# Performance work log

Hardware: AMD Instinct MI355X
Metric: run time of the kernel (lower is better)

Reference implementation:

```python
import jax, jax.numpy as jnp
import numpy as np

N_NODES = 20000
N_EDGES = 320000
NFEAT = 50
ALPHA = 0.2  # leaky relu slope
EPS = 1e-16


def _gat_head(x, src, dst, W, a, concat):
    # x: (N, Fin), W: (Fin, Fout), a: (2*Fout,)
    N = x.shape[0]
    Wh = x @ W                      # (N, Fout)
    Fout = W.shape[1]
    # edge_h @ a == Wh[src] @ a[:Fout] + Wh[dst] @ a[Fout:]
    s_src = Wh @ a[:Fout]           # (N,)
    s_dst = Wh @ a[Fout:]           # (N,)
    e = jax.nn.leaky_relu(s_src[src] + s_dst[dst], negative_slope=ALPHA)  # (E,)
    # segment softmax over incoming edges of each target node
    e_max = jax.ops.segment_max(e, dst, num_segments=N)   # (N,)
    e_exp = jnp.exp(e - e_max[dst])                         # (E,)
    e_sum = jax.ops.segment_sum(e_exp, dst, num_segments=N)
    att = e_exp / (e_sum[dst] + EPS)                        # (E,)
    msg = Wh[src] * att[:, None]                            # (E, Fout)
    h = jax.ops.segment_sum(msg, dst, num_segments=N)       # (N, Fout)
    return jax.nn.elu(h) if concat else h


def _multi_head(x, src, dst, W, a, concat):
    # W: (H, Fin, Fout), a: (H, 2*Fout) -> (H, N, Fout)
    return jax.vmap(_gat_head, in_axes=(None, None, None, 0, 0, None))(x, src, dst, W, a, concat)


def setup_inputs() -> dict:
    key = jax.random.key(0)
    ks = jax.random.split(key, 8)
    x = jax.random.normal(ks[0], (N_NODES, NFEAT), dtype=jnp.float32)
    edge_index = jax.random.randint(ks[1], (2, N_EDGES), 0, N_NODES, dtype=jnp.int64)
    s = 0.1
    W1 = jax.random.normal(ks[2], (4, NFEAT, 256), dtype=jnp.float32) * s
    a1 = jax.random.normal(ks[3], (4, 512), dtype=jnp.float32) * s
    W2 = jax.random.normal(ks[4], (4, 1024, 256), dtype=jnp.float32) * s
    a2 = jax.random.normal(ks[5], (4, 512), dtype=jnp.float32) * s
    W3 = jax.random.normal(ks[6], (6, 1024, 121), dtype=jnp.float32) * s
    a3 = jax.random.normal(ks[7], (6, 242), dtype=jnp.float32) * s
    return {"x": x, "edge_index": edge_index, "W1": W1, "a1": a1, "W2": W2, "a2": a2, "W3": W3, "a3": a3}


def reference(x, edge_index, W1, a1, W2, a2, W3, a3):
    src, dst = edge_index[0], edge_index[1]
    N = x.shape[0]
    # layer 1: 4 heads, concat -> (N, 1024), then elu
    h1 = _multi_head(x, src, dst, W1, a1, True)      # (4, N, 256)
    x1 = jnp.transpose(h1, (1, 0, 2)).reshape(N, -1)  # concat along feature dim
    x1 = jax.nn.elu(x1)
    # layer 2: 4 heads, concat + skip connection, then elu
    h2 = _multi_head(x1, src, dst, W2, a2, True)
    x2 = jnp.transpose(h2, (1, 0, 2)).reshape(N, -1)
    x2 = jax.nn.elu(x2 + x1)
    # layer 3: 6 heads, no concat-elu, mean over heads
    h3 = _multi_head(x2, src, dst, W3, a3, False)     # (6, N, 121)
    x3 = jnp.mean(h3, axis=0)
    return jax.nn.sigmoid(x3)
```

## Files before the change

kernel.cpp:

```cpp
#include <hip/hip_runtime.h>
#include <cstdint>

#define N_NODES 20000
#define N_EDGES 320000
#define ALPHA 0.2f
#define GAT_EPS 1e-16f
#define MPAD 20096
#define RBLK 157
#define RHI 20
#define SCAN_BLKS 80
#define BT_ROWS 1152

typedef __attribute__((ext_vector_type(8))) _Float16 half8;
typedef __attribute__((ext_vector_type(4))) _Float16 half4t;
typedef __attribute__((ext_vector_type(16))) float f32x16;
typedef __attribute__((ext_vector_type(2))) float f32x2;

__device__ __forceinline__ float elu1(float x) { return x > 0.f ? x : __expf(x) - 1.f; }

__device__ __forceinline__ unsigned char f2fp8(float x) {
    return (unsigned char)(__builtin_amdgcn_cvt_pk_fp8_f32(x, 0.f, 0, false) & 0xff);
}

__device__ __forceinline__ void async16(const void* g, void* l) {
    __builtin_amdgcn_global_load_lds(
        (const __attribute__((address_space(1))) unsigned int*)g,
        (__attribute__((address_space(3))) unsigned int*)l, 16, 0, 0);
}

__device__ __forceinline__ float rdlanef(float v, int j) {
    return __int_as_float(__builtin_amdgcn_readlane(__float_as_int(v), j));
}

__global__ void hist_kernel(const int* __restrict__ dst, int* __restrict__ counts, int E) {
    int e = blockIdx.x * blockDim.x + threadIdx.x;
    if (e < E) atomicAdd(&counts[dst[e]], 1);
}

__global__ void scan1_kernel(const int* __restrict__ counts, int* __restrict__ excl,
                             int* __restrict__ partial, int N) {
    __shared__ int sh[256];
    int t = threadIdx.x, b = blockIdx.x;
    int i = b * 256 + t;
    int v = (i < N) ? counts[i] : 0;
    sh[t] = v;
    __syncthreads();
    for (int d = 1; d < 256; d <<= 1) {
        int x = (t >= d) ? sh[t - d] : 0;
        __syncthreads();
        sh[t] += x;
        __syncthreads();
    }
    if (i < N) excl[i] = sh[t] - v;
    if (t == 255) partial[b] = sh[255];
}

__global__ void scan2_kernel(int* __restrict__ partial) {
    __shared__ int sh[128];
    int t = threadIdx.x;
    int v = (t < SCAN_BLKS) ? partial[t] : 0;
    sh[t] = v;
    __syncthreads();
    for (int d = 1; d < 128; d <<= 1) {
        int x = (t >= d) ? sh[t - d] : 0;
        __syncthreads();
        sh[t] += x;
        __syncthreads();
    }
    if (t < SCAN_BLKS) partial[t] = sh[t] - v;
}

__global__ void scan3_kernel(const int* __restrict__ excl, const int* __restrict__ partial,
                             int* __restrict__ rowptr, int* __restrict__ cursor, int N, int E) {
    int t = threadIdx.x, b = blockIdx.x;
    int i = b * 256 + t;
    if (i < N) {
        int v = excl[i] + partial[b];
        rowptr[i] = v;
        cursor[i] = v;
    }
    if (i == 0) rowptr[N] = E;
}

__global__ void scatter_kernel(const int* __restrict__ src, const int* __restrict__ dst,
                               int* __restrict__ cursor, int* __restrict__ esrc, int E) {
    int e = blockIdx.x * blockDim.x + threadIdx.x;
    if (e < E) {
        int p = atomicAdd(&cursor[dst[e]], 1);
        esrc[p] = src[e];
    }
}

__global__ void pack_x16(const float* __restrict__ x, _Float16* __restrict__ A) {
    int idx = blockIdx.x * 256 + threadIdx.x;
    int r = idx >> 6, c = idx & 63;
    float v = (r < N_NODES && c < 50) ? x[r * 50 + c] : 0.f;
    A[idx] = (_Float16)v;
}

__global__ void pack_bt1(const float* __restrict__ W, _Float16* __restrict__ Bt) {
    int idx = blockIdx.x * 256 + threadIdx.x;
    int c = idx >> 6, k = idx & 63;
    int h = c >> 8, f = c & 255;
    float v = (k < 50) ? W[((size_t)h * 50 + k) * 256 + f] : 0.f;
    Bt[idx] = (_Float16)v;
}

__global__ void pack_bt16(const float* __restrict__ W, _Float16* __restrict__ Bt,
                          int F, int Fpad, int Ctot) {
    int c = blockIdx.y;
    int k = blockIdx.x * blockDim.x + threadIdx.x;
    float v = 0.f;
    if (c < Ctot) {
        int h = c / Fpad, f = c - h * Fpad;
        if (f < F) v = W[(size_t)h * 1024 * F + (size_t)k * F + f];
    }
    Bt[(size_t)c * 1024 + k] = (_Float16)v;
}

__global__ __launch_bounds__(64) void wtilde_kernel(const float* __restrict__ W,
                                                    const float* __restrict__ a,
                                                    _Float16* __restrict__ BT, int Kreal,
                                                    int Kdim, int F, int H, int Nfeat) {
    int k = blockIdx.x, j = blockIdx.y;
    if (j >= 2 * H) return;
    int lane = threadIdx.x;
    int h = j < H ? j : j - H;
    int ao = j < H ? 0 : F;
    float s = 0.f;
    if (k < Kreal) {
        const float* wp = W + ((size_t)h * Kreal + k) * F;
        const float* ap = a + (size_t)h * 2 * F + ao;
        for (int f = lane; f < F; f += 64) s += wp[f] * ap[f];
    }
#pragma unroll
    for (int off = 32; off; off >>= 1) s += __shfl_down(s, off);
    if (lane == 0) BT[(size_t)(Nfeat + j) * Kdim + k] = (_Float16)s;
}

__global__ __launch_bounds__(256) void gemm_f16(const _Float16* __restrict__ A,
                                                const _Float16* __restrict__ BT,
                                                unsigned char* __restrict__ C8,
                                                float* __restrict__ SPRE,
                                                int M, int Nfeat, int ld, int Kdim, int Cblk) {
    int id = blockIdx.x;
    int xm = id & 7, q = id >> 3;
    int cb = q % Cblk, rh = q / Cblk;
    int rb = rh * 8 + xm;
    if (rb >= RBLK) return;
    __shared__ __align__(16) _Float16 sA[2][128 * 64];
    __shared__ __align__(16) _Float16 sB[2][128 * 64];
    int t = threadIdx.x;
    int row0 = rb * 128, col0 = cb * 128;
    int lane = t & 63, wave = t >> 6;
    int wm = wave >> 1, wn = wave & 1;
    int l31 = lane & 31;
    int lhi = lane >> 5;

    const _Float16* gA = A + (size_t)row0 * Kdim;
    const _Float16* gB = BT + (size_t)col0 * Kdim;

    int sR[4], sgl[4];
#pragma unroll
    for (int i = 0; i < 4; i++) {
        int m = i * 256 + t;
        sR[i] = m >> 3;
        sgl[i] = (m & 7) ^ (sR[i] & 7);
    }

    f32x16 acc[2][2] = {};

#pragma unroll
    for (int i = 0; i < 4; i++) {
        const _Float16* pa = gA + (size_t)sR[i] * Kdim + sgl[i] * 8;
        const _Float16* pb = gB + (size_t)sR[i] * Kdim + sgl[i] * 8;
        async16(pa, &sA[0][(i * 256 + t) * 8]);
        async16(pb, &sB[0][(i * 256 + t) * 8]);
    }

    int cur = 0;
    for (int k0 = 0; k0 < Kdim; k0 += 64) {
        __syncthreads();
        int nxt = k0 + 64;
        if (nxt < Kdim) {
            int nb = cur ^ 1;
#pragma unroll
            for (int i = 0; i < 4; i++) {
                const _Float16* pa = gA + (size_t)sR[i] * Kdim + nxt + sgl[i] * 8;
                const _Float16* pb = gB + (size_t)sR[i] * Kdim + nxt + sgl[i] * 8;
                async16(pa, &sA[nb][(i * 256 + t) * 8]);
                async16(pb, &sB[nb][(i * 256 + t) * 8]);
            }
        }
        const _Float16* cA = sA[cur];
        const _Float16* cB = sB[cur];
#pragma unroll
        for (int kk = 0; kk < 4; kk++) {
            int g = kk * 2 + lhi;
            half8 af[2], bf[2];
#pragma unroll
            for (int mt = 0; mt < 2; mt++) {
                int R = wm * 64 + mt * 32 + l31;
                int gp = g ^ (R & 7);
                af[mt] = *(const half8*)(cA + R * 64 + gp * 8);
            }
#pragma unroll
            for (int nt = 0; nt < 2; nt++) {
                int R = wn * 64 + nt * 32 + l31;
                int gp = g ^ (R & 7);
                bf[nt] = *(const half8*)(cB + R * 64 + gp * 8);
            }
#pragma unroll
            for (int mt = 0; mt < 2; mt++)
#pragma unroll
                for (int nt = 0; nt < 2; nt++)
                    acc[mt][nt] = __builtin_amdgcn_mfma_f32_32x32x16_f16(af[mt], bf[nt], acc[mt][nt], 0, 0, 0);
        }
        cur ^= 1;
    }

    int cb32 = col0 + wn * 64 + l31;
    int rb32 = row0 + wm * 64 + 4 * lhi;
#pragma unroll
    for (int mt = 0; mt < 2; mt++)
#pragma unroll
        for (int nt = 0; nt < 2; nt++) {
            int gc = cb32 + nt * 32;
            if (gc < Nfeat) {
#pragma unroll
                for (int r = 0; r < 16; r++) {
                    int gr = rb32 + mt * 32 + (r & 3) + 8 * (r >> 2);
                    if (gr < M) C8[(size_t)gr * ld + gc] = f2fp8(acc[mt][nt][r]);
                }
            } else if (gc < Nfeat + 12) {
                int j = gc - Nfeat;
#pragma unroll
                for (int r = 0; r < 16; r++) {
                    int gr = rb32 + mt * 32 + (r & 3) + 8 * (r >> 2);
                    if (gr < M) SPRE[(size_t)j * N_NODES + gr] = acc[mt][nt][r];
                }
            }
        }
}

__global__ __launch_bounds__(256) void attagg256_kernel(const int* __restrict__ rowptr,
                                                        const int* __restrict__ esrc,
                                                        const float* __restrict__ SPRE,
                                                        const unsigned char* __restrict__ WH8,
                                                        _Float16* __restrict__ X16,
                                                        int use_skip, int N) {
    int n = blockIdx.x;
    int h = threadIdx.x >> 6;
    int lane = threadIdx.x & 63;
    int start = rowptr[n], end = rowptr[n + 1];
    const float* ss = SPRE + (size_t)h * N;
    float sd = SPRE[(size_t)(4 + h) * N + n];

    float m = -1e30f, s = 0.f;
    int sidx = 0; float ssc = -1e30f;
    for (int e0 = start; e0 < end; e0 += 64) {
        int e = e0 + lane;
        bool act = e < end;
        int idx = act ? esrc[e] : 0;
        float sc = -1e30f;
        if (act) {
            sc = ss[idx] + sd;
            sc = sc > 0.f ? sc : ALPHA * sc;
        }
        sidx = idx; ssc = sc;
        float mn = fmaxf(m, sc);
        s = s * __expf(m - mn) + (act ? __expf(sc - mn) : 0.f);
        m = mn;
    }
    float lm = m;
#pragma unroll
    for (int off = 1; off < 64; off <<= 1) m = fmaxf(m, __shfl_xor(m, off));
    float ptil = s * __expf(lm - m);
    s = ptil;
#pragma unroll
    for (int off = 1; off < 64; off <<= 1) s += __shfl_xor(s, off);
    float inv = 1.f / (s + GAT_EPS);
    bool single = (end - start) <= 64;

    const unsigned char* Wb = WH8 + h * 256 + lane * 4;
    float a0 = 0.f, a1 = 0.f, a2 = 0.f, a3 = 0.f;
    int lastStart = start + (((end - start - 1) >> 6) << 6);
    for (int e0 = start; e0 < end; e0 += 64) {
        int e = e0 + lane;
        bool act = e < end;
        int idx; float p;
        if (e0 == lastStart) {
            idx = sidx;
            p = act ? (single ? ptil * inv : __expf(ssc - m) * inv) : 0.f;
        } else {
            idx = act ? esrc[e] : 0;
            float sc = -1e30f;
            if (act) {
                sc = ss[idx] + sd;
                sc = sc > 0.f ? sc : ALPHA * sc;
            }
            p = act ? __expf(sc - m) * inv : 0.f;
        }
        int cnt = end - e0; if (cnt > 64) cnt = 64;
        int j = 0;
        for (; j + 4 <= cnt; j += 4) {
            int i0 = __builtin_amdgcn_readlane(idx, j);
            int i1 = __builtin_amdgcn_readlane(idx, j + 1);
            int i2 = __builtin_amdgcn_readlane(idx, j + 2);
            int i3 = __builtin_amdgcn_readlane(idx, j + 3);
            float p0 = rdlanef(p, j), p1 = rdlanef(p, j + 1);
            float p2 = rdlanef(p, j + 2), p3 = rdlanef(p, j + 3);
            unsigned int w0 = *(const unsigned int*)(Wb + (size_t)i0 * 1024);
            unsigned int w1 = *(const unsigned int*)(Wb + (size_t)i1 * 1024);
            unsigned int w2 = *(const unsigned int*)(Wb + (size_t)i2 * 1024);
            unsigned int w3 = *(const unsigned int*)(Wb + (size_t)i3 * 1024);
            f32x2 l0 = __builtin_amdgcn_cvt_pk_f32_fp8((int)w0, false);
            f32x2 h0v = __builtin_amdgcn_cvt_pk_f32_fp8((int)w0, true);
            f32x2 l1 = __builtin_amdgcn_cvt_pk_f32_fp8((int)w1, false);
            f32x2 h1v = __builtin_amdgcn_cvt_pk_f32_fp8((int)w1, true);
            f32x2 l2 = __builtin_amdgcn_cvt_pk_f32_fp8((int)w2, false);
            f32x2 h2v = __builtin_amdgcn_cvt_pk_f32_fp8((int)w2, true);
            f32x2 l3 = __builtin_amdgcn_cvt_pk_f32_fp8((int)w3, false);
            f32x2 h3v = __builtin_amdgcn_cvt_pk_f32_fp8((int)w3, true);
            a0 += p0 * l0.x + p1 * l1.x + p2 * l2.x + p3 * l3.x;
            a1 += p0 * l0.y + p1 * l1.y + p2 * l2.y + p3 * l3.y;
            a2 += p0 * h0v.x + p1 * h1v.x + p2 * h2v.x + p3 * h3v.x;
            a3 += p0 * h0v.y + p1 * h1v.y + p2 * h2v.y + p3 * h3v.y;
        }
        for (; j < cnt; j++) {
            int ij = __builtin_amdgcn_readlane(idx, j);
            float pj = rdlanef(p, j);
            unsigned int w = *(const unsigned int*)(Wb + (size_t)ij * 1024);
            f32x2 lo = __builtin_amdgcn_cvt_pk_f32_fp8((int)w, false);
            f32x2 hi = __builtin_amdgcn_cvt_pk_f32_fp8((int)w, true);
            a0 += pj * lo.x; a1 += pj * lo.y; a2 += pj * hi.x; a3 += pj * hi.y;
        }
    }

    size_t o = (size_t)n * 1024 + h * 256 + lane * 4;
    float v0, v1, v2, v3;
    if (use_skip) {
        half4t sk = *(const half4t*)(X16 + o);
        v0 = elu1(elu1(a0) + (float)sk.x);
        v1 = elu1(elu1(a1) + (float)sk.y);
        v2 = elu1(elu1(a2) + (float)sk.z);
        v3 = elu1(elu1(a3) + (float)sk.w);
    } else {
        v0 = elu1(elu1(a0)); v1 = elu1(elu1(a1));
        v2 = elu1(elu1(a2)); v3 = elu1(elu1(a3));
    }
    half4t r;
    r.x = (_Float16)v0; r.y = (_Float16)v1; r.z = (_Float16)v2; r.w = (_Float16)v3;
    *(half4t*)(X16 + o) = r;
}

__global__ __launch_bounds__(384) void attagg726_kernel(const int* __restrict__ rowptr,
                                                        const int* __restrict__ esrc,
                                                        const float* __restrict__ SPRE,
                                                        const unsigned char* __restrict__ WH8,
                                                        float* __restrict__ out, int N) {
    __shared__ float part[6][124];
    int n = blockIdx.x;
    int t = threadIdx.x;
    int h = t >> 6;
    int lane = t & 63;
    int start = rowptr[n], end = rowptr[n + 1];
    const float* ss = SPRE + (size_t)h * N;
    float sd = SPRE[(size_t)(6 + h) * N + n];

    float m = -1e30f, s = 0.f;
    int sidx = 0; float ssc = -1e30f;
    for (int e0 = start; e0 < end; e0 += 64) {
        int e = e0 + lane;
        bool act = e < end;
        int idx = act ? esrc[e] : 0;
        float sc = -1e30f;
        if (act) {
            sc = ss[idx] + sd;
            sc = sc > 0.f ? sc : ALPHA * sc;
        }
        sidx = idx; ssc = sc;
        float mn = fmaxf(m, sc);
        s = s * __expf(m - mn) + (act ? __expf(sc - mn) : 0.f);
        m = mn;
    }
    float lm = m;
#pragma unroll
    for (int off = 1; off < 64; off <<= 1) m = fmaxf(m, __shfl_xor(m, off));
    float ptil = s * __expf(lm - m);
    s = ptil;
#pragma unroll
    for (int off = 1; off < 64; off <<= 1) s += __shfl_xor(s, off);
    float inv = 1.f / (s + GAT_EPS);
    bool single = (end - start) <= 64;

    const unsigned char* Wb = WH8 + h * 124 + 2 * lane;
    float a0 = 0.f, a1 = 0.f;
    int lastStart = start + (((end - start - 1) >> 6) << 6);
    for (int e0 = start; e0 < end; e0 += 64) {
        int e = e0 + lane;
        bool act = e < end;
        int idx; float p;
        if (e0 == lastStart) {
            idx = sidx;
            p = act ? (single ? ptil * inv : __expf(ssc - m) * inv) : 0.f;
        } else {
            idx = act ? esrc[e] : 0;
            float sc = -1e30f;
            if (act) {
                sc = ss[idx] + sd;
                sc = sc > 0.f ? sc : ALPHA * sc;
            }
            p = act ? __expf(sc - m) * inv : 0.f;
        }
        int cnt = end - e0; if (cnt > 64) cnt = 64;
        if (lane < 62) {
            int j = 0;
            for (; j + 4 <= cnt; j += 4) {
                int i0 = __builtin_amdgcn_readlane(idx, j);
                int i1 = __builtin_amdgcn_readlane(idx, j + 1);
                int i2 = __builtin_amdgcn_readlane(idx, j + 2);
                int i3 = __builtin_amdgcn_readlane(idx, j + 3);
                float p0 = rdlanef(p, j), p1 = rdlanef(p, j + 1);
                float p2 = rdlanef(p, j + 2), p3 = rdlanef(p, j + 3);
                unsigned short w0 = *(const unsigned short*)(Wb + (size_t)i0 * 768);
                unsigned short w1 = *(const unsigned short*)(Wb + (size_t)i1 * 768);
                unsigned short w2 = *(const unsigned short*)(Wb + (size_t)i2 * 768);
                unsigned short w3 = *(const unsigned short*)(Wb + (size_t)i3 * 768);
                f32x2 f0 = __builtin_amdgcn_cvt_pk_f32_fp8((int)w0, false);
                f32x2 f1 = __builtin_amdgcn_cvt_pk_f32_fp8((int)w1, false);
                f32x2 f2 = __builtin_amdgcn_cvt_pk_f32_fp8((int)w2, false);
                f32x2 f3 = __builtin_amdgcn_cvt_pk_f32_fp8((int)w3, false);
                a0 += p0 * f0.x + p1 * f1.x + p2 * f2.x + p3 * f3.x;
                a1 += p0 * f0.y + p1 * f1.y + p2 * f2.y + p3 * f3.y;
            }
            for (; j < cnt; j++) {
                int ij = __builtin_amdgcn_readlane(idx, j);
                float pj = rdlanef(p, j);
                unsigned short w = *(const unsigned short*)(Wb + (size_t)ij * 768);
                f32x2 f = __builtin_amdgcn_cvt_pk_f32_fp8((int)w, false);
                a0 += pj * f.x; a1 += pj * f.y;
            }
        }
    }
    if (lane < 62) {
        part[h][2 * lane]     = a0;
        part[h][2 * lane + 1] = a1;
    }
    __syncthreads();
    if (t < 121) {
        float tot = (part[0][t] + part[1][t] + part[2][t] +
                     part[3][t] + part[4][t] + part[5][t]) * (1.f / 6.f);
        out[(size_t)n * 121 + t] = 1.f / (1.f + __expf(-tot));
    }
}

extern "C" void kernel_launch(void* const* d_in, const int* in_sizes, int n_in,
                              void* d_out, int out_size, void* d_ws, size_t ws_size,
                              hipStream_t stream) {
    const float* x  = (const float*)d_in[0];
    const int*   ei = (const int*)d_in[1];
    const float* W1 = (const float*)d_in[2];
    const float* a1 = (const float*)d_in[3];
    const float* W2 = (const float*)d_in[4];
    const float* a2 = (const float*)d_in[5];
    const float* W3 = (const float*)d_in[6];
    const float* a3 = (const float*)d_in[7];
    float* out = (float*)d_out;
    const int N = N_NODES, E = N_EDGES;
    const int* src = ei;
    const int* dst = ei + E;

    char* ws = (char*)d_ws;
    size_t off = 0;
    auto alloc = [&](size_t b) { size_t o = off; off += (b + 255) & ~(size_t)255; return o; };
    _Float16* X16  = (_Float16*)(ws + alloc((size_t)MPAD * 1024 * 2));
    unsigned char* WH8 = (unsigned char*)(ws + alloc((size_t)MPAD * 1024));
    _Float16* BT16 = (_Float16*)(ws + alloc((size_t)BT_ROWS * 1024 * 2));
    _Float16* A1   = (_Float16*)(ws + alloc((size_t)MPAD * 64 * 2));
    _Float16* BT1  = (_Float16*)(ws + alloc((size_t)BT_ROWS * 64 * 2));
    float* SPRE   = (float*)(ws + alloc((size_t)12 * N * 4));
    int*   rowptr = (int*)(ws + alloc((size_t)(N + 1) * 4));
    int*   cursor = (int*)(ws + alloc((size_t)N * 4));
    int*   counts = (int*)(ws + alloc((size_t)N * 4));
    int*   excl   = (int*)(ws + alloc((size_t)N * 4));
    int*   partial= (int*)(ws + alloc((size_t)SCAN_BLKS * 4));
    int*   esrc   = (int*)(ws + alloc((size_t)E * 4));

    hipMemsetAsync(counts, 0, (size_t)N * 4, stream);
    hist_kernel<<<(E + 255) / 256, 256, 0, stream>>>(dst, counts, E);
    scan1_kernel<<<SCAN_BLKS, 256, 0, stream>>>(counts, excl, partial, N);
    scan2_kernel<<<1, 128, 0, stream>>>(partial);
    scan3_kernel<<<SCAN_BLKS, 256, 0, stream>>>(excl, partial, rowptr, cursor, N, E);
    scatter_kernel<<<(E + 255) / 256, 256, 0, stream>>>(src, dst, cursor, esrc, E);
    hipMemsetAsync(X16 + (size_t)N * 1024, 0, (size_t)(MPAD - N) * 1024 * 2, stream);

    pack_x16<<<MPAD * 64 / 256, 256, 0, stream>>>(x, A1);
    pack_bt1<<<1024 * 64 / 256, 256, 0, stream>>>(W1, BT1);
    wtilde_kernel<<<dim3(64, 8), 64, 0, stream>>>(W1, a1, BT1, 50, 64, 256, 4, 1024);
    gemm_f16<<<8 * RHI * 9, 256, 0, stream>>>(A1, BT1, WH8, SPRE, N, 1024, 1024, 64, 9);
    attagg256_kernel<<<N, 256, 0, stream>>>(rowptr, esrc, SPRE, WH8, X16, 0, N);

    pack_bt16<<<dim3(4, 1024), 256, 0, stream>>>(W2, BT16, 256, 256, 1024);
    wtilde_kernel<<<dim3(1024, 8), 64, 0, stream>>>(W2, a2, BT16, 1024, 1024, 256, 4, 1024);
    gemm_f16<<<8 * RHI * 9, 256, 0, stream>>>(X16, BT16, WH8, SPRE, N, 1024, 1024, 1024, 9);
    attagg256_kernel<<<N, 256, 0, stream>>>(rowptr, esrc, SPRE, WH8, X16, 1, N);

    pack_bt16<<<dim3(4, 744), 256, 0, stream>>>(W3, BT16, 121, 124, 744);
    wtilde_kernel<<<dim3(1024, 12), 64, 0, stream>>>(W3, a3, BT16, 1024, 1024, 121, 6, 744);
    gemm_f16<<<8 * RHI * 6, 256, 0, stream>>>(X16, BT16, WH8, SPRE, N, 744, 768, 1024, 6);
    attagg726_kernel<<<N, 384, 0, stream>>>(rowptr, esrc, SPRE, WH8, out, N);
}
```

Measured before the change: 462.9 us.

## Add single-chunk fast path with software-pipelined fp8 gathers in attention aggregation

```diff
diff --git a/kernel.cpp b/kernel.cpp
--- a/kernel.cpp
+++ b/kernel.cpp
@@ -253,87 +253,137 @@
     int h = threadIdx.x >> 6;
     int lane = threadIdx.x & 63;
     int start = rowptr[n], end = rowptr[n + 1];
+    int cnt = end - start;
     const float* ss = SPRE + (size_t)h * N;
     float sd = SPRE[(size_t)(4 + h) * N + n];
-
-    float m = -1e30f, s = 0.f;
-    int sidx = 0; float ssc = -1e30f;
-    for (int e0 = start; e0 < end; e0 += 64) {
-        int e = e0 + lane;
+    const unsigned char* Wb = WH8 + h * 256 + lane * 4;
+    float a0 = 0.f, a1 = 0.f, a2 = 0.f, a3 = 0.f;
+
+    if (cnt <= 64) {
+        int e = start + lane;
         bool act = e < end;
         int idx = act ? esrc[e] : 0;
+
+        unsigned int wA[8], wB[8], wC[8];
+        auto ISSUE = [&](unsigned int (&buf)[8], int base) {
+#pragma unroll
+            for (int u = 0; u < 8; u++) {
+                int ij = __builtin_amdgcn_readlane(idx, base + u);
+                buf[u] = *(const unsigned int*)(Wb + ((size_t)(unsigned)ij << 10));
+            }
+        };
+        ISSUE(wA, 0);
+        if (cnt > 8) ISSUE(wB, 8);
+        if (cnt > 16) ISSUE(wC, 16);
+
         float sc = -1e30f;
         if (act) {
             sc = ss[idx] + sd;
             sc = sc > 0.f ? sc : ALPHA * sc;
         }
-        sidx = idx; ssc = sc;
-        float mn = fmaxf(m, sc);
-        s = s * __expf(m - mn) + (act ? __expf(sc - mn) : 0.f);
-        m = mn;
-    }
-    float lm = m;
-#pragma unroll
-    for (int off = 1; off < 64; off <<= 1) m = fmaxf(m, __shfl_xor(m, off));
-    float ptil = s * __expf(lm - m);
-    s = ptil;
-#pragma unroll
-    for (int off = 1; off < 64; off <<= 1) s += __shfl_xor(s, off);
-    float inv = 1.f / (s + GAT_EPS);
-    bool single = (end - start) <= 64;
-
-    const unsigned char* Wb = WH8 + h * 256 + lane * 4;
-    float a0 = 0.f, a1 = 0.f, a2 = 0.f, a3 = 0.f;
-    int lastStart = start + (((end - start - 1) >> 6) << 6);
-    for (int e0 = start; e0 < end; e0 += 64) {
-        int e = e0 + lane;
-        bool act = e < end;
-        int idx; float p;
-        if (e0 == lastStart) {
-            idx = sidx;
-            p = act ? (single ? ptil * inv : __expf(ssc - m) * inv) : 0.f;
-        } else {
-            idx = act ? esrc[e] : 0;
+        float m = sc;
+#pragma unroll
+        for (int off = 1; off < 64; off <<= 1) m = fmaxf(m, __shfl_xor(m, off));
+        float ptil = act ? __expf(sc - m) : 0.f;
+        float s = ptil;
+#pragma unroll
+        for (int off = 1; off < 64; off <<= 1) s += __shfl_xor(s, off);
+        float p = ptil * (1.f / (s + GAT_EPS));
+
+        auto CONSUME = [&](unsigned int (&buf)[8], int base) {
+#pragma unroll
+            for (int u = 0; u < 8; u++) {
+                float pj = rdlanef(p, base + u);
+                f32x2 lo = __builtin_amdgcn_cvt_pk_f32_fp8((int)buf[u], false);
+                f32x2 hi = __builtin_amdgcn_cvt_pk_f32_fp8((int)buf[u], true);
+                a0 += pj * lo.x; a1 += pj * lo.y; a2 += pj * hi.x; a3 += pj * hi.y;
+            }
+        };
+        CONSUME(wA, 0);
+        if (cnt > 8)  { if (cnt > 24) ISSUE(wA, 24); CONSUME(wB, 8); }
+        if (cnt > 16) { if (cnt > 32) ISSUE(wB, 32); CONSUME(wC, 16); }
+        if (cnt > 24) { if (cnt > 40) ISSUE(wC, 40); CONSUME(wA, 24); }
+        if (cnt > 32) { if (cnt > 48) ISSUE(wA, 48); CONSUME(wB, 32); }
+        if (cnt > 40) { if (cnt > 56) ISSUE(wB, 56); CONSUME(wC, 40); }
+        if (cnt > 48) CONSUME(wA, 48);
+        if (cnt > 56) CONSUME(wB, 56);
+    } else {
+        float m = -1e30f, s = 0.f;
+        int sidx = 0; float ssc = -1e30f;
+        for (int e0 = start; e0 < end; e0 += 64) {
+            int e = e0 + lane;
+            bool act = e < end;
+            int idx = act ? esrc[e] : 0;
             float sc = -1e30f;
             if (act) {
                 sc = ss[idx] + sd;
                 sc = sc > 0.f ? sc : ALPHA * sc;
             }
-            p = act ? __expf(sc - m) * inv : 0.f;
-        }
-        int cnt = end - e0; if (cnt > 64) cnt = 64;
-        int j = 0;
-        for (; j + 4 <= cnt; j += 4) {
-            int i0 = __builtin_amdgcn_readlane(idx, j);
-            int i1 = __builtin_amdgcn_readlane(idx, j + 1);
-            int i2 = __builtin_amdgcn_readlane(idx, j + 2);
-            int i3 = __builtin_amdgcn_readlane(idx, j + 3);
-            float p0 = rdlanef(p, j), p1 = rdlanef(p, j + 1);
-            float p2 = rdlanef(p, j + 2), p3 = rdlanef(p, j + 3);
-            unsigned int w0 = *(const unsigned int*)(Wb + (size_t)i0 * 1024);
-            unsigned int w1 = *(const unsigned int*)(Wb + (size_t)i1 * 1024);
-            unsigned int w2 = *(const unsigned int*)(Wb + (size_t)i2 * 1024);
-            unsigned int w3 = *(const unsigned int*)(Wb + (size_t)i3 * 1024);
-            f32x2 l0 = __builtin_amdgcn_cvt_pk_f32_fp8((int)w0, false);
-            f32x2 h0v = __builtin_amdgcn_cvt_pk_f32_fp8((int)w0, true);
-            f32x2 l1 = __builtin_amdgcn_cvt_pk_f32_fp8((int)w1, false);
-            f32x2 h1v = __builtin_amdgcn_cvt_pk_f32_fp8((int)w1, true);
-            f32x2 l2 = __builtin_amdgcn_cvt_pk_f32_fp8((int)w2, false);
-            f32x2 h2v = __builtin_amdgcn_cvt_pk_f32_fp8((int)w2, true);
-            f32x2 l3 = __builtin_amdgcn_cvt_pk_f32_fp8((int)w3, false);
-            f32x2 h3v = __builtin_amdgcn_cvt_pk_f32_fp8((int)w3, true);
-            a0 += p0 * l0.x + p1 * l1.x + p2 * l2.x + p3 * l3.x;
-            a1 += p0 * l0.y + p1 * l1.y + p2 * l2.y + p3 * l3.y;
-            a2 += p0 * h0v.x + p1 * h1v.x + p2 * h2v.x + p3 * h3v.x;
-            a3 += p0 * h0v.y + p1 * h1v.y + p2 * h2v.y + p3 * h3v.y;
-        }
-        for (; j < cnt; j++) {
-            int ij = __builtin_amdgcn_readlane(idx, j);
-            float pj = rdlanef(p, j);
-            unsigned int w = *(const unsigned int*)(Wb + (size_t)ij * 1024);
-            f32x2 lo = __builtin_amdgcn_cvt_pk_f32_fp8((int)w, false);
-            f32x2 hi = __builtin_amdgcn_cvt_pk_f32_fp8((int)w, true);
-            a0 += pj * lo.x; a1 += pj * lo.y; a2 += pj * hi.x; a3 += pj * hi.y;
+            sidx = idx; ssc = sc;
+            float mn = fmaxf(m, sc);
+            s = s * __expf(m - mn) + (act ? __expf(sc - mn) : 0.f);
+            m = mn;
+        }
+        float lm = m;
+#pragma unroll
+        for (int off = 1; off < 64; off <<= 1) m = fmaxf(m, __shfl_xor(m, off));
+        float ptil = s * __expf(lm - m);
+        s = ptil;
+#pragma unroll
+        for (int off = 1; off < 64; off <<= 1) s += __shfl_xor(s, off);
+        float inv = 1.f / (s + GAT_EPS);
+
+        int lastStart = start + (((end - start - 1) >> 6) << 6);
+        for (int e0 = start; e0 < end; e0 += 64) {
+            int e = e0 + lane;
+            bool act = e < end;
+            int idx; float p;
+            if (e0 == lastStart) {
+                idx = sidx;
+                p = act ? __expf(ssc - m) * inv : 0.f;
+            } else {
+                idx = act ? esrc[e] : 0;
+                float sc = -1e30f;
+                if (act) {
+                    sc = ss[idx] + sd;
+                    sc = sc > 0.f ? sc : ALPHA * sc;
+                }
+                p = act ? __expf(sc - m) * inv : 0.f;
+            }
+            int cn = end - e0; if (cn > 64) cn = 64;
+            int j = 0;
+            for (; j + 4 <= cn; j += 4) {
+                int i0 = __builtin_amdgcn_readlane(idx, j);
+                int i1 = __builtin_amdgcn_readlane(idx, j + 1);
+                int i2 = __builtin_amdgcn_readlane(idx, j + 2);
+                int i3 = __builtin_amdgcn_readlane(idx, j + 3);
+                float p0 = rdlanef(p, j), p1 = rdlanef(p, j + 1);
+                float p2 = rdlanef(p, j + 2), p3 = rdlanef(p, j + 3);
+                unsigned int w0 = *(const unsigned int*)(Wb + (size_t)i0 * 1024);
+                unsigned int w1 = *(const unsigned int*)(Wb + (size_t)i1 * 1024);
+                unsigned int w2 = *(const unsigned int*)(Wb + (size_t)i2 * 1024);
+                unsigned int w3 = *(const unsigned int*)(Wb + (size_t)i3 * 1024);
+                f32x2 l0 = __builtin_amdgcn_cvt_pk_f32_fp8((int)w0, false);
+                f32x2 h0v = __builtin_amdgcn_cvt_pk_f32_fp8((int)w0, true);
+                f32x2 l1 = __builtin_amdgcn_cvt_pk_f32_fp8((int)w1, false);
+                f32x2 h1v = __builtin_amdgcn_cvt_pk_f32_fp8((int)w1, true);
+                f32x2 l2 = __builtin_amdgcn_cvt_pk_f32_fp8((int)w2, false);
+                f32x2 h2v = __builtin_amdgcn_cvt_pk_f32_fp8((int)w2, true);
+                f32x2 l3 = __builtin_amdgcn_cvt_pk_f32_fp8((int)w3, false);
+                f32x2 h3v = __builtin_amdgcn_cvt_pk_f32_fp8((int)w3, true);
+                a0 += p0 * l0.x + p1 * l1.x + p2 * l2.x + p3 * l3.x;
+                a1 += p0 * l0.y + p1 * l1.y + p2 * l2.y + p3 * l3.y;
+                a2 += p0 * h0v.x + p1 * h1v.x + p2 * h2v.x + p3 * h3v.x;
+                a3 += p0 * h0v.y + p1 * h1v.y + p2 * h2v.y + p3 * h3v.y;
+            }
+            for (; j < cn; j++) {
+                int ij = __builtin_amdgcn_readlane(idx, j);
+                float pj = rdlanef(p, j);
+                unsigned int w = *(const unsigned int*)(Wb + (size_t)ij * 1024);
+                f32x2 lo = __builtin_amdgcn_cvt_pk_f32_fp8((int)w, false);
+                f32x2 hi = __builtin_amdgcn_cvt_pk_f32_fp8((int)w, true);
+                a0 += pj * lo.x; a1 += pj * lo.y; a2 += pj * hi.x; a3 += pj * hi.y;
+            }
         }
     }
 
@@ -365,58 +415,105 @@
     int h = t >> 6;
     int lane = t & 63;
     int start = rowptr[n], end = rowptr[n + 1];
+    int cnt = end - start;
     const float* ss = SPRE + (size_t)h * N;
     float sd = SPRE[(size_t)(6 + h) * N + n];
-
-    float m = -1e30f, s = 0.f;
-    int sidx = 0; float ssc = -1e30f;
-    for (int e0 = start; e0 < end; e0 += 64) {
-        int e = e0 + lane;
+    const unsigned char* Wb = WH8 + h * 124 + 2 * lane;
+    float a0 = 0.f, a1 = 0.f;
+
+    if (cnt <= 64) {
+        int e = start + lane;
         bool act = e < end;
         int idx = act ? esrc[e] : 0;
+
+        unsigned short wA[8], wB[8], wC[8];
+        auto ISSUE = [&](unsigned short (&buf)[8], int base) {
+#pragma unroll
+            for (int u = 0; u < 8; u++) {
+                int ij = __builtin_amdgcn_readlane(idx, base + u);
+                buf[u] = *(const unsigned short*)(Wb + (size_t)(unsigned)ij * 768u);
+            }
+        };
+        ISSUE(wA, 0);
+        if (cnt > 8) ISSUE(wB, 8);
+        if (cnt > 16) ISSUE(wC, 16);
+
         float sc = -1e30f;
         if (act) {
             sc = ss[idx] + sd;
             sc = sc > 0.f ? sc : ALPHA * sc;
         }
-        sidx = idx; ssc = sc;
-        float mn = fmaxf(m, sc);
-        s = s * __expf(m - mn) + (act ? __expf(sc - mn) : 0.f);
-        m = mn;
-    }
-    float lm = m;
-#pragma unroll
-    for (int off = 1; off < 64; off <<= 1) m = fmaxf(m, __shfl_xor(m, off));
-    float ptil = s * __expf(lm - m);
-    s = ptil;
-#pragma unroll
-    for (int off = 1; off < 64; off <<= 1) s += __shfl_xor(s, off);
-    float inv = 1.f / (s + GAT_EPS);
-    bool single = (end - start) <= 64;
-
-    const unsigned char* Wb = WH8 + h * 124 + 2 * lane;
-    float a0 = 0.f, a1 = 0.f;
-    int lastStart = start + (((end - start - 1) >> 6) << 6);
-    for (int e0 = start; e0 < end; e0 += 64) {
-        int e = e0 + lane;
-        bool act = e < end;
-        int idx; float p;
-        if (e0 == lastStart) {
-            idx = sidx;
-            p = act ? (single ? ptil * inv : __expf(ssc - m) * inv) : 0.f;
-        } else {
-            idx = act ? esrc[e] : 0;
+        float m = sc;
+#pragma unroll
+        for (int off = 1; off < 64; off <<= 1) m = fmaxf(m, __shfl_xor(m, off));
+        float ptil = act ? __expf(sc - m) : 0.f;
+        float s = ptil;
+#pragma unroll
+        for (int off = 1; off < 64; off <<= 1) s += __shfl_xor(s, off);
+        float p = ptil * (1.f / (s + GAT_EPS));
+
+        auto CONSUME = [&](unsigned short (&buf)[8], int base) {
+#pragma unroll
+            for (int u = 0; u < 8; u++) {
+                float pj = rdlanef(p, base + u);
+                f32x2 f = __builtin_amdgcn_cvt_pk_f32_fp8((int)buf[u], false);
+                a0 += pj * f.x; a1 += pj * f.y;
+            }
+        };
+        CONSUME(wA, 0);
+        if (cnt > 8)  { if (cnt > 24) ISSUE(wA, 24); CONSUME(wB, 8); }
+        if (cnt > 16) { if (cnt > 32) ISSUE(wB, 32); CONSUME(wC, 16); }
+        if (cnt > 24) { if (cnt > 40) ISSUE(wC, 40); CONSUME(wA, 24); }
+        if (cnt > 32) { if (cnt > 48) ISSUE(wA, 48); CONSUME(wB, 32); }
+        if (cnt > 40) { if (cnt > 56) ISSUE(wB, 56); CONSUME(wC, 40); }
+        if (cnt > 48) CONSUME(wA, 48);
+        if (cnt > 56) CONSUME(wB, 56);
+    } else {
+        float m = -1e30f, s = 0.f;
+        int sidx = 0; float ssc = -1e30f;
+        for (int e0 = start; e0 < end; e0 += 64) {
+            int e = e0 + lane;
+            bool act = e < end;
+            int idx = act ? esrc[e] : 0;
             float sc = -1e30f;
             if (act) {
                 sc = ss[idx] + sd;
                 sc = sc > 0.f ? sc : ALPHA * sc;
             }
-            p = act ? __expf(sc - m) * inv : 0.f;
-        }
-        int cnt = end - e0; if (cnt > 64) cnt = 64;
-        if (lane < 62) {
+            sidx = idx; ssc = sc;
+            float mn = fmaxf(m, sc);
+            s = s * __expf(m - mn) + (act ? __expf(sc - mn) : 0.f);
+            m = mn;
+        }
+        float lm = m;
+#pragma unroll
+        for (int off = 1; off < 64; off <<= 1) m = fmaxf(m, __shfl_xor(m, off));
+        float ptil = s * __expf(lm - m);
+        s = ptil;
+#pragma unroll
+        for (int off = 1; off < 64; off <<= 1) s += __shfl_xor(s, off);
+        float inv = 1.f / (s + GAT_EPS);
+
+        int lastStart = start + (((end - start - 1) >> 6) << 6);
+        for (int e0 = start; e0 < end; e0 += 64) {
+            int e = e0 + lane;
+            bool act = e < end;
+            int idx; float p;
+            if (e0 == lastStart) {
+                idx = sidx;
+                p = act ? __expf(ssc - m) * inv : 0.f;
+            } else {
+                idx = act ? esrc[e] : 0;
+                float sc = -1e30f;
+                if (act) {
+                    sc = ss[idx] + sd;
+                    sc = sc > 0.f ? sc : ALPHA * sc;
+                }
+                p = act ? __expf(sc - m) * inv : 0.f;
+            }
+            int cn = end - e0; if (cn > 64) cn = 64;
             int j = 0;
-            for (; j + 4 <= cnt; j += 4) {
+            for (; j + 4 <= cn; j += 4) {
                 int i0 = __builtin_amdgcn_readlane(idx, j);
                 int i1 = __builtin_amdgcn_readlane(idx, j + 1);
                 int i2 = __builtin_amdgcn_readlane(idx, j + 2);
@@ -434,7 +531,7 @@
                 a0 += p0 * f0.x + p1 * f1.x + p2 * f2.x + p3 * f3.x;
                 a1 += p0 * f0.y + p1 * f1.y + p2 * f2.y + p3 * f3.y;
             }
-            for (; j < cnt; j++) {
+            for (; j < cn; j++) {
                 int ij = __builtin_amdgcn_readlane(idx, j);
                 float pj = rdlanef(p, j);
                 unsigned short w = *(const unsigned short*)(Wb + (size_t)ij * 768);
@@ -443,6 +540,7 @@
             }
         }
     }
+
     if (lane < 62) {
         part[h][2 * lane]     = a0;
         part[h][2 * lane + 1] = a1;
```

Result: faster. 448.5 us (-3.1%).
